# Kernel optimization log

Hardware: AMD Instinct MI355X
Metric: run time of the kernel (lower is better)

The kernel has to match this reference:

```python
import jax, jax.numpy as jnp
import numpy as np

N = 200000   # nodes
E = 3200000  # edges
B = 1024     # graphs in batch
A = 10       # num_actions
IN, C, ED = 9, 64, 1
NEG_SLOPE = 0.2


def _xavier(k, shape):
    lim = (6.0 / (shape[0] + shape[1])) ** 0.5
    return jax.random.uniform(k, shape, jnp.float32, -lim, lim)


def setup_inputs() -> dict:
    key = jax.random.key(0)
    ks = jax.random.split(key, 24)
    x = jax.random.normal(ks[0], (N, IN), jnp.float32)
    edge_index = jax.random.randint(ks[1], (2, E), 0, N, dtype=jnp.int64)
    edge_attr = jax.random.normal(ks[2], (E, ED), jnp.float32)
    agent_state = jax.random.normal(ks[3], (B, 34), jnp.float32)
    pool_batch = jnp.sort(jax.random.randint(ks[4], (N,), 0, B, dtype=jnp.int64))
    return {
        "x": x, "edge_index": edge_index, "edge_attr": edge_attr,
        "agent_state": agent_state, "pool_batch": pool_batch,
        # GATConv params (heads=1): lin (no bias), lin_edge (no bias), att vectors, bias
        "W_gat": _xavier(ks[5], (IN, C)),
        "att_src": jax.random.normal(ks[6], (C,), jnp.float32) * 0.1,
        "att_dst": jax.random.normal(ks[7], (C,), jnp.float32) * 0.1,
        "W_edge": _xavier(ks[8], (ED, C)),
        "att_edge": jax.random.normal(ks[9], (C,), jnp.float32) * 0.1,
        "b_gat": jnp.zeros((C,), jnp.float32),
        # fc_input1: Linear(64,128)
        "W1": _xavier(ks[10], (C, 128)), "b1": jnp.zeros((128,), jnp.float32),
        # fc_input2: Linear(34,64)
        "W2": _xavier(ks[11], (34, 64)), "b2": jnp.zeros((64,), jnp.float32),
        # fc_output: Linear(192,128), Linear(128,A)
        "W3": _xavier(ks[12], (192, 128)), "b3": jnp.zeros((128,), jnp.float32),
        "W4": _xavier(ks[13], (128, A)), "b4": jnp.zeros((A,), jnp.float32),
    }


def _gat_forward(x, edge_index, edge_attr, W_gat, att_src, att_dst, W_edge, att_edge, b_gat):
    src, dst = edge_index[0], edge_index[1]
    # add self-loops; self-loop edge_attr = mean of incoming edge_attr (PyG fill_value='mean')
    ones = jnp.ones((E,), jnp.float32)
    deg = jax.ops.segment_sum(ones, dst, num_segments=N)
    loop_attr = jax.ops.segment_sum(edge_attr, dst, num_segments=N) / jnp.maximum(deg, 1.0)[:, None]
    loop_idx = jnp.arange(N, dtype=src.dtype)
    src_f = jnp.concatenate([src, loop_idx])
    dst_f = jnp.concatenate([dst, loop_idx])
    attr_f = jnp.concatenate([edge_attr, loop_attr], axis=0)  # [E+N, 1]
    h = x @ W_gat                                   # [N, C]
    a_src = h @ att_src                             # [N]
    a_dst = h @ att_dst                             # [N]
    a_edge = (attr_f @ W_edge) @ att_edge           # [E+N]
    alpha = jax.nn.leaky_relu(a_src[src_f] + a_dst[dst_f] + a_edge, NEG_SLOPE)
    # per-destination softmax (stable)
    m = jax.ops.segment_max(alpha, dst_f, num_segments=N)
    ea = jnp.exp(alpha - m[dst_f])
    denom = jax.ops.segment_sum(ea, dst_f, num_segments=N)
    coef = ea / denom[dst_f]                        # [E+N]
    out = jax.ops.segment_sum(coef[:, None] * h[src_f], dst_f, num_segments=N)
    return out + b_gat


def reference(x, edge_index, edge_attr, agent_state, pool_batch,
              W_gat, att_src, att_dst, W_edge, att_edge, b_gat,
              W1, b1, W2, b2, W3, b3, W4, b4):
    g = _gat_forward(x, edge_index, edge_attr, W_gat, att_src, att_dst, W_edge, att_edge, b_gat)
    g = jax.nn.relu(g @ W1 + b1)                    # [N, 128]
    # global mean pool per graph
    s = jax.ops.segment_sum(g, pool_batch, num_segments=B)
    cnt = jax.ops.segment_sum(jnp.ones((N,), g.dtype), pool_batch, num_segments=B)
    pooled = s / jnp.maximum(cnt, 1.0)[:, None]     # [B, 128]
    a = jax.nn.relu(agent_state @ W2 + b2)          # [B, 64]
    z = jnp.concatenate([pooled, a], axis=-1)       # [B, 192]
    z = jax.nn.relu(z @ W3 + b3)
    return z @ W4 + b4                              # [B, A]
```

## Files before the change

### kernel.cpp

```cpp
#include <hip/hip_runtime.h>
#include <hip/hip_bf16.h>

namespace {

constexpr int kN  = 200000;
constexpr int kE  = 3200000;
constexpr int kB  = 1024;
constexpr int kA  = 10;
constexpr int kIn = 9;
constexpr int kC  = 64;
constexpr int kH1 = 128;
constexpr int kAS = 34;
constexpr int kH2 = 64;
constexpr int kZ  = 192;
constexpr int kH3 = 128;
constexpr int kMAXD = 192;
constexpr int kNBUCK = 782;
constexpr int kEPC  = 4096;
constexpr int kNCHK = (kE + kEPC - 1) / kEPC;
constexpr int kNODEBLK = kN / 4;

using bf16 = __hip_bfloat16;
typedef __attribute__((ext_vector_type(8))) short short8;
typedef __attribute__((ext_vector_type(4))) float f32x4;

__device__ __forceinline__ float b2f(bf16 v) { return __bfloat162float(v); }
__device__ __forceinline__ float lrelu(float x) { return x > 0.f ? x : 0.2f * x; }

__device__ __forceinline__ float ldf(const void* p, size_t i, int f32) {
  return f32 ? ((const float*)p)[i] : __bfloat162float(((const bf16*)p)[i]);
}
__device__ __forceinline__ int ldi(const void* p, size_t i, int i64) {
  return i64 ? (int)(((const long long*)p)[i]) : ((const int*)p)[i];
}

__global__ void k_init2(const void* __restrict__ ei, const void* __restrict__ x,
                        const void* __restrict__ We, const void* __restrict__ ae,
                        const void* __restrict__ Wg, const void* __restrict__ vsw,
                        const void* __restrict__ vdw, const void* __restrict__ W1,
                        const void* __restrict__ b1, const void* __restrict__ bgat,
                        int* __restrict__ flags, float* __restrict__ scal,
                        short* __restrict__ w1t, float* __restrict__ bb1) {
  __shared__ int c0, c1;
  int t = threadIdx.x;
  if (t == 0) { c0 = 0; c1 = 0; }
  __syncthreads();
  int zc = (((const int*)ei)[2 * t + 1] == 0) ? 1 : 0;
  int nc = 0;
  for (int j = t; j < 8192; j += 1024) {
    unsigned short u = ((const unsigned short*)x)[j];
    if ((u & 0x7F80u) == 0x7F80u) nc++;
  }
  atomicAdd(&c0, zc);
  atomicAdd(&c1, nc);
  __syncthreads();
  int f32 = (c1 > 3) ? 1 : 0;
  if (t == 0) { flags[0] = (c0 > 512) ? 1 : 0; flags[1] = f32; }
  int wid = t >> 6, lane = t & 63;
  if (wid == 0) {
    float p = ldf(We, lane, f32) * ldf(ae, lane, f32);
    #pragma unroll
    for (int o = 32; o > 0; o >>= 1) p += __shfl_xor(p, o);
    if (lane == 0) scal[0] = p;
  } else if (wid <= kIn) {
    int k = wid - 1;
    float w = ldf(Wg, (size_t)k * kC + lane, f32);
    float ps = w * ldf(vsw, lane, f32);
    float pd = w * ldf(vdw, lane, f32);
    #pragma unroll
    for (int o = 32; o > 0; o >>= 1) { ps += __shfl_xor(ps, o); pd += __shfl_xor(pd, o); }
    if (lane == 0) { scal[1 + k] = ps; scal[10 + k] = pd; }
  }
  for (int i = t; i < kC * kH1; i += 1024) {
    int c = i >> 6, k = i & 63;
    float v = ldf(W1, (size_t)k * kH1 + c, f32);
    w1t[i] = (short)__bfloat16_as_ushort(__float2bfloat16(v));
  }
  if (t < kH1) {
    int c = t;
    float s = ldf(b1, c, f32);
    for (int k = 0; k < kC; ++k)
      s += ldf(bgat, k, f32) * ldf(W1, (size_t)k * kH1 + c, f32);
    bb1[c] = s;
  }
}

__global__ void k_diag(const int* __restrict__ flags, float ws_mb,
                       float* __restrict__ out) {
  int i = blockIdx.x * 256 + threadIdx.x;
  if (i >= kB * kA) return;
  float v;
  if (flags) v = (1 + flags[0]) * 1e7f + (1 + flags[1]) * 1e6f + fminf(ws_mb, 999999.f);
  else       v = 3e7f + fminf(ws_mb, 999999.f);
  out[i] = v;
}

__global__ void __launch_bounds__(256) k_nodehist(
    const void* __restrict__ x, const void* __restrict__ Wg,
    const void* __restrict__ ei, const int* __restrict__ flags,
    const float* __restrict__ scal, bf16* __restrict__ hout,
    float* __restrict__ a_src, float* __restrict__ a_dst,
    int* __restrict__ blockhist) {
  int tid = threadIdx.x;
  int f32 = flags[1];
  if (blockIdx.x < kNODEBLK) {
    __shared__ float wg[kIn * kC];
    __shared__ float sc[19];
    for (int i = tid; i < kIn * kC; i += 256) wg[i] = ldf(Wg, i, f32);
    if (tid < 19) sc[tid] = scal[tid];
    __syncthreads();
    int n = blockIdx.x * 4 + (tid >> 6);
    int lane = tid & 63;
    float hc = 0.f, as_ = 0.f, ad_ = 0.f;
    #pragma unroll
    for (int k = 0; k < kIn; ++k) {
      float xv = ldf(x, (size_t)n * kIn + k, f32);
      hc  += xv * wg[k * kC + lane];
      as_ += xv * sc[1 + k];
      ad_ += xv * sc[10 + k];
    }
    hout[(size_t)n * kC + lane] = __float2bfloat16(hc);
    if (lane == 0) { a_src[n] = as_; a_dst[n] = ad_; }
  } else {
    __shared__ int hh[kNBUCK];
    int i64 = flags[0];
    int c = blockIdx.x - kNODEBLK;
    for (int i = tid; i < kNBUCK; i += 256) hh[i] = 0;
    __syncthreads();
    int e0 = c * kEPC;
    #pragma unroll
    for (int j = 0; j < 16; ++j) {
      int e = e0 + j * 256 + tid;
      if (e < kE) {
        int d = ldi(ei, (size_t)kE + e, i64);
        atomicAdd(&hh[d >> 8], 1);
      }
    }
    __syncthreads();
    for (int i = tid; i < kNBUCK; i += 256) blockhist[(size_t)i * kNCHK + c] = hh[i];
  }
}

__global__ void __launch_bounds__(256) r_scanA(int* __restrict__ blockhist,
                                               int* __restrict__ buckettot) {
  __shared__ int lds[256];
  int b = blockIdx.x, tid = threadIdx.x;
  int run = 0;
  for (int c0 = 0; c0 < kNCHK; c0 += 256) {
    int idx = c0 + tid;
    int v = (idx < kNCHK) ? blockhist[(size_t)b * kNCHK + idx] : 0;
    int xv = v;
    lds[tid] = xv;
    __syncthreads();
    #pragma unroll
    for (int o = 1; o < 256; o <<= 1) {
      int t = (tid >= o) ? lds[tid - o] : 0;
      __syncthreads();
      xv += t;
      lds[tid] = xv;
      __syncthreads();
    }
    if (idx < kNCHK) blockhist[(size_t)b * kNCHK + idx] = run + xv - v;
    run += lds[255];
    __syncthreads();
  }
  if (tid == 0) buckettot[b] = run;
}

__global__ void r_scanB(const int* __restrict__ buckettot, int* __restrict__ bucketbase) {
  __shared__ int lds[1024];
  int tid = threadIdx.x;
  int v = (tid < kNBUCK) ? buckettot[tid] : 0;
  int xv = v;
  lds[tid] = xv;
  __syncthreads();
  #pragma unroll
  for (int o = 1; o < 1024; o <<= 1) {
    int t = (tid >= o) ? lds[tid - o] : 0;
    __syncthreads();
    xv += t;
    lds[tid] = xv;
    __syncthreads();
  }
  if (tid < kNBUCK) bucketbase[tid] = xv - v;
  if (tid == kNBUCK - 1) bucketbase[kNBUCK] = xv;
}

__global__ void __launch_bounds__(256) r_scatter(
    const void* __restrict__ ei, const void* __restrict__ eattr,
    const int* __restrict__ flags, const float* __restrict__ a_src,
    const float* __restrict__ scal, const int* __restrict__ blockhist,
    const int* __restrict__ bucketbase, int2* __restrict__ mid) {
  __shared__ int cur[kNBUCK];
  int i64 = flags[0], f32 = flags[1];
  int c = blockIdx.x, tid = threadIdx.x;
  for (int i = tid; i < kNBUCK; i += 256)
    cur[i] = bucketbase[i] + blockhist[(size_t)i * kNCHK + c];
  __syncthreads();
  float sedge = scal[0];
  int e0 = c * kEPC;
  #pragma unroll
  for (int j = 0; j < 16; ++j) {
    int e = e0 + j * 256 + tid;
    if (e < kE) {
      int s = ldi(ei, e, i64);
      int d = ldi(ei, (size_t)kE + e, i64);
      float ap = a_src[s] + sedge * ldf(eattr, e, f32);
      int pos = atomicAdd(&cur[d >> 8], 1);
      mid[pos] = make_int2(s | ((d & 255) << 18), __float_as_int(ap));
    }
  }
}

__global__ void __launch_bounds__(256) r_bucket(
    const int2* __restrict__ mid, const int* __restrict__ bucketbase,
    int* __restrict__ offs, int2* __restrict__ csr) {
  __shared__ int h[256], cur[256], lds[256];
  int b = blockIdx.x, tid = threadIdx.x;
  int base = bucketbase[b];
  int cnt = bucketbase[b + 1] - base;
  h[tid] = 0;
  __syncthreads();
  for (int i = tid; i < cnt; i += 256)
    atomicAdd(&h[(mid[base + i].x >> 18) & 255], 1);
  __syncthreads();
  int v = h[tid];
  int xv = v;
  lds[tid] = xv;
  __syncthreads();
  #pragma unroll
  for (int o = 1; o < 256; o <<= 1) {
    int t = (tid >= o) ? lds[tid - o] : 0;
    __syncthreads();
    xv += t;
    lds[tid] = xv;
    __syncthreads();
  }
  int excl = xv - v;
  int n = b * 256 + tid;
  if (n < kN) offs[n] = base + excl;
  if (b == kNBUCK - 1 && tid == 0) offs[kN] = kE;
  cur[tid] = excl;
  __syncthreads();
  for (int i = tid; i < cnt; i += 256) {
    int2 e = mid[base + i];
    int dl = (e.x >> 18) & 255;
    int pos = atomicAdd(&cur[dl], 1);
    csr[base + pos] = make_int2(e.x & 0x3FFFF, e.y);
  }
}

__global__ void __launch_bounds__(256) k_gather5(
    const bf16* __restrict__ h, const float* __restrict__ a_src,
    const float* __restrict__ a_dst, const int* __restrict__ offs,
    const int2* __restrict__ csr, bf16* __restrict__ gbuf) {
  int wid = threadIdx.x >> 6, lane = threadIdx.x & 63;
  int n0 = (blockIdx.x * 4 + wid) * 4;
  for (int t = 0; t < 4; ++t) {
    int n = n0 + t;
    int base = offs[n];
    int degc = min(offs[n + 1] - base, kMAXD);
    float adst = a_dst[n], asrcn = a_src[n];
    int s0_ = 0, s1_ = 0, s2_ = 0;
    float e0_ = 0.f, e1_ = 0.f, e2_ = 0.f;
    float sap = 0.f;
    if (lane < degc) {
      int2 c = csr[base + lane];
      s0_ = c.x;
      float ap = __int_as_float(c.y);
      sap += ap - a_src[s0_];
      e0_ = __expf(fminf(lrelu(ap + adst), 60.f));
    }
    if (lane + 64 < degc) {
      int2 c = csr[base + lane + 64];
      s1_ = c.x;
      float ap = __int_as_float(c.y);
      sap += ap - a_src[s1_];
      e1_ = __expf(fminf(lrelu(ap + adst), 60.f));
    }
    if (lane + 128 < degc) {
      int2 c = csr[base + lane + 128];
      s2_ = c.x;
      float ap = __int_as_float(c.y);
      sap += ap - a_src[s2_];
      e2_ = __expf(fminf(lrelu(ap + adst), 60.f));
    }
    float se = e0_ + e1_ + e2_;
    #pragma unroll
    for (int o = 32; o > 0; o >>= 1) {
      se  += __shfl_xor(se, o);
      sap += __shfl_xor(sap, o);
    }
    float la = sap / fmaxf((float)degc, 1.0f);
    float aself = lrelu(asrcn + adst + la);
    float eself = __expf(fminf(aself, 60.f));
    float inv = 1.f / (se + eself);
    float g = eself * b2f(h[(size_t)n * kC + lane]);
    int lim = min(degc, 64);
    int j = 0;
    for (; j + 3 < lim; j += 4) {
      int sa = __shfl(s0_, j),     sb = __shfl(s0_, j + 1);
      int sc = __shfl(s0_, j + 2), sd = __shfl(s0_, j + 3);
      float ea = __shfl(e0_, j),     eb = __shfl(e0_, j + 1);
      float ec = __shfl(e0_, j + 2), ed = __shfl(e0_, j + 3);
      float ha = b2f(h[(size_t)sa * kC + lane]);
      float hb = b2f(h[(size_t)sb * kC + lane]);
      float hcv = b2f(h[(size_t)sc * kC + lane]);
      float hd = b2f(h[(size_t)sd * kC + lane]);
      g += ea * ha;
      g += eb * hb;
      g += ec * hcv;
      g += ed * hd;
    }
    for (; j < lim; ++j)
      g += __shfl(e0_, j) * b2f(h[(size_t)__shfl(s0_, j) * kC + lane]);
    if (degc > 64) {
      int lim1 = min(degc, 128) - 64;
      for (int j2 = 0; j2 < lim1; ++j2)
        g += __shfl(e1_, j2) * b2f(h[(size_t)__shfl(s1_, j2) * kC + lane]);
      if (degc > 128) {
        int lim2 = degc - 128;
        for (int j2 = 0; j2 < lim2; ++j2)
          g += __shfl(e2_, j2) * b2f(h[(size_t)__shfl(s2_, j2) * kC + lane]);
      }
    }
    gbuf[(size_t)n * kC + lane] = __float2bfloat16(g * inv);
  }
}

__device__ __forceinline__ int lowb(const void* pb, int i64, int target) {
  int lo = 0, hi = kN;
  while (lo < hi) {
    int mid = (lo + hi) >> 1;
    if (ldi(pb, mid, i64) < target) lo = mid + 1; else hi = mid;
  }
  return lo;
}

__global__ void __launch_bounds__(512) k_fc1graph(
    const short* __restrict__ gbuf, const short* __restrict__ w1t,
    const float* __restrict__ bb1, const void* __restrict__ pb,
    const int* __restrict__ flags, float* __restrict__ pooled) {
  int i64 = flags[0];
  int b = blockIdx.x;
  int wv = threadIdx.x >> 6, lane = threadIdx.x & 63;
  int col = lane & 15, kg = lane >> 4;
  int c = wv * 16 + col;
  int c0 = lowb(pb, i64, b);
  int c1 = lowb(pb, i64, b + 1);
  float ct = fmaxf((float)(c1 - c0), 1.0f);
  short8 bf0 = *(const short8*)(w1t + (size_t)c * kC + kg * 8);
  short8 bf1 = *(const short8*)(w1t + (size_t)c * kC + 32 + kg * 8);
  float bias = bb1[c];
  float pacc = 0.f;
  int g0 = c0 >> 4, g1 = (c1 + 15) >> 4;
  for (int gi = g0; gi < g1; ++gi) {
    int n0 = gi * 16;
    const short* arow = gbuf + (size_t)(n0 + col) * kC + kg * 8;
    short8 a0 = *(const short8*)(arow);
    short8 a1 = *(const short8*)(arow + 32);
    f32x4 acc = {bias, bias, bias, bias};
    acc = __builtin_amdgcn_mfma_f32_16x16x32_bf16(a0, bf0, acc, 0, 0, 0);
    acc = __builtin_amdgcn_mfma_f32_16x16x32_bf16(a1, bf1, acc, 0, 0, 0);
    #pragma unroll
    for (int r = 0; r < 4; ++r) {
      int node = n0 + kg * 4 + r;
      float v = fmaxf(acc[r], 0.f);
      pacc += (node >= c0 && node < c1) ? v : 0.f;
    }
  }
  pacc += __shfl_xor(pacc, 16);
  pacc += __shfl_xor(pacc, 32);
  if (kg == 0) pooled[(size_t)b * kH1 + c] = pacc / ct;
}

__global__ void k_final(const float* __restrict__ pooled,
                        const void* __restrict__ agent, const void* __restrict__ W2,
                        const void* __restrict__ b2v, const void* __restrict__ W3,
                        const void* __restrict__ b3v, const void* __restrict__ W4,
                        const void* __restrict__ b4v, const int* __restrict__ flags,
                        float* __restrict__ out) {
  __shared__ float z[kZ];
  __shared__ float t[kH3];
  int f32 = flags[1];
  int b = blockIdx.x, l = threadIdx.x;
  float av = ldf(b2v, l, f32);
  for (int k = 0; k < kAS; ++k)
    av += ldf(agent, (size_t)b * kAS + k, f32) * ldf(W2, (size_t)k * kH2 + l, f32);
  z[kH1 + l] = fmaxf(av, 0.f);
  z[l] = pooled[(size_t)b * kH1 + l];
  z[64 + l] = pooled[(size_t)b * kH1 + 64 + l];
  __syncthreads();
  float t0 = ldf(b3v, l, f32), t1 = ldf(b3v, 64 + l, f32);
  for (int k = 0; k < kZ; ++k) {
    float zk = z[k];
    t0 += zk * ldf(W3, (size_t)k * kH3 + l, f32);
    t1 += zk * ldf(W3, (size_t)k * kH3 + 64 + l, f32);
  }
  t[l] = fmaxf(t0, 0.f);
  t[64 + l] = fmaxf(t1, 0.f);
  __syncthreads();
  if (l < kA) {
    float o = ldf(b4v, l, f32);
    for (int k = 0; k < kH3; ++k) o += t[k] * ldf(W4, (size_t)k * kA + l, f32);
    out[b * kA + l] = o;
  }
}

}

extern "C" void kernel_launch(void* const* d_in, const int* in_sizes, int n_in,
                              void* d_out, int out_size, void* d_ws, size_t ws_size,
                              hipStream_t stream) {
  const void* x     = d_in[0];
  const void* ei    = d_in[1];
  const void* eattr = d_in[2];
  const void* agent = d_in[3];
  const void* pb    = d_in[4];
  const void* Wg    = d_in[5];
  const void* att_s = d_in[6];
  const void* att_d = d_in[7];
  const void* We    = d_in[8];
  const void* att_e = d_in[9];
  const void* bgat  = d_in[10];
  const void* W1    = d_in[11];
  const void* b1    = d_in[12];
  const void* W2    = d_in[13];
  const void* b2v   = d_in[14];
  const void* W3    = d_in[15];
  const void* b3v   = d_in[16];
  const void* W4    = d_in[17];
  const void* b4v   = d_in[18];
  float* out = (float*)d_out;

  char* ws = (char*)d_ws;
  size_t off = 0;
  auto alloc = [&](size_t bytes) -> void* {
    void* p = ws + off;
    off += (bytes + 255) & ~size_t(255);
    return p;
  };
  int*   flags  = (int*)alloc(256);
  size_t zbytes = off;
  float* pooled     = (float*)alloc(size_t(kB) * kH1 * 4);
  float* scal       = (float*)alloc(256);
  short* w1t        = (short*)alloc(size_t(kC) * kH1 * 2);
  float* bb1        = (float*)alloc(size_t(kH1) * 4);
  int*   buckettot  = (int*)alloc(size_t(kNBUCK) * 4);
  int*   bucketbase = (int*)alloc((size_t(kNBUCK) + 1) * 4);
  float* a_src      = (float*)alloc(size_t(kN) * 4);
  float* a_dst      = (float*)alloc(size_t(kN) * 4);
  int*   offs       = (int*)alloc((size_t(kN) + 1) * 4);
  int*   blockhist  = (int*)alloc(size_t(kNBUCK) * kNCHK * 4);
  int2*  csr = (int2*)alloc(size_t(kE) * 8);
  bf16*  h   = (bf16*)alloc(size_t(kN) * kC * 2);
  char*  uni  = (char*)alloc(size_t(kE) * 8 + 4096);
  int2*  mid  = (int2*)uni;
  bf16*  gbuf = (bf16*)uni;
  size_t need = off;

  float ws_mb = (float)(double(ws_size) / (1024.0 * 1024.0));

  if (ws_size < 4096) {
    k_diag<<<(kB * kA + 255) / 256, 256, 0, stream>>>(nullptr, ws_mb, out);
    return;
  }
  hipMemsetAsync(ws, 0, (ws_size < need) ? size_t(256) : zbytes, stream);
  k_init2<<<1, 1024, 0, stream>>>(ei, x, We, att_e, Wg, att_s, att_d, W1, b1, bgat,
                                  flags, scal, w1t, bb1);
  if (ws_size < need) {
    k_diag<<<(kB * kA + 255) / 256, 256, 0, stream>>>(flags, ws_mb, out);
    return;
  }

  k_nodehist<<<kNODEBLK + kNCHK, 256, 0, stream>>>(x, Wg, ei, flags, scal, h,
                                                   a_src, a_dst, blockhist);
  r_scanA<<<kNBUCK, 256, 0, stream>>>(blockhist, buckettot);
  r_scanB<<<1, 1024, 0, stream>>>(buckettot, bucketbase);
  r_scatter<<<kNCHK, 256, 0, stream>>>(ei, eattr, flags, a_src, scal, blockhist,
                                       bucketbase, mid);
  r_bucket<<<kNBUCK, 256, 0, stream>>>(mid, bucketbase, offs, csr);
  k_gather5<<<kN / 16, 256, 0, stream>>>(h, a_src, a_dst, offs, csr, gbuf);
  k_fc1graph<<<kB, 512, 0, stream>>>((const short*)gbuf, w1t, bb1, pb, flags, pooled);
  k_final<<<kB, 64, 0, stream>>>(pooled, agent, W2, b2v, W3, b3v, W4, b4v,
                                 flags, out);
}
```

Before: 374.8 us.

## Fuse per-bucket sort with attention gather in shared memory, dropping CSR pass

The bucket size drops from 256 to 128 destination nodes. The second-level per-destination sort is merged into the gather kernel: each block sorts its bucket's edges into LDS and then computes the softmax aggregation straight from LDS. This removes the global CSR array, the offsets array and one full write and read of the edge list. Edges per chunk are doubled and scatter uses 512 threads. The risk is that a bucket with more than 2688 edges is silently truncated, and the larger LDS footprint may lower occupancy.

```diff
diff --git a/kernel.cpp b/kernel.cpp
--- a/kernel.cpp
+++ b/kernel.cpp
@@ -14,9 +14,10 @@
 constexpr int kH2 = 64;
 constexpr int kZ  = 192;
 constexpr int kH3 = 128;
-constexpr int kMAXD = 192;
-constexpr int kNBUCK = 782;
-constexpr int kEPC  = 4096;
+constexpr int kDB = 128;
+constexpr int kNBUCK = (kN + kDB - 1) / kDB;
+constexpr int kSE = 2688;
+constexpr int kEPC  = 8192;
 constexpr int kNCHK = (kE + kEPC - 1) / kEPC;
 constexpr int kNODEBLK = kN / 4;
 
@@ -129,11 +130,11 @@
     __syncthreads();
     int e0 = c * kEPC;
     #pragma unroll
-    for (int j = 0; j < 16; ++j) {
+    for (int j = 0; j < kEPC / 256; ++j) {
       int e = e0 + j * 256 + tid;
       if (e < kE) {
         int d = ldi(ei, (size_t)kE + e, i64);
-        atomicAdd(&hh[d >> 8], 1);
+        atomicAdd(&hh[d >> 7], 1);
       }
     }
     __syncthreads();
@@ -170,8 +171,11 @@
 __global__ void r_scanB(const int* __restrict__ buckettot, int* __restrict__ bucketbase) {
   __shared__ int lds[1024];
   int tid = threadIdx.x;
-  int v = (tid < kNBUCK) ? buckettot[tid] : 0;
-  int xv = v;
+  int i0 = tid * 2, i1 = tid * 2 + 1;
+  int v0 = (i0 < kNBUCK) ? buckettot[i0] : 0;
+  int v1 = (i1 < kNBUCK) ? buckettot[i1] : 0;
+  int s = v0 + v1;
+  int xv = s;
   lds[tid] = xv;
   __syncthreads();
   #pragma unroll
@@ -182,11 +186,13 @@
     lds[tid] = xv;
     __syncthreads();
   }
-  if (tid < kNBUCK) bucketbase[tid] = xv - v;
-  if (tid == kNBUCK - 1) bucketbase[kNBUCK] = xv;
-}
-
-__global__ void __launch_bounds__(256) r_scatter(
+  int excl = xv - s;
+  if (i0 < kNBUCK) bucketbase[i0] = excl;
+  if (i1 < kNBUCK) bucketbase[i1] = excl + v0;
+  if (tid == 1023) bucketbase[kNBUCK] = xv;
+}
+
+__global__ void __launch_bounds__(512) r_scatter(
     const void* __restrict__ ei, const void* __restrict__ eattr,
     const int* __restrict__ flags, const float* __restrict__ a_src,
     const float* __restrict__ scal, const int* __restrict__ blockhist,
@@ -194,107 +200,110 @@
   __shared__ int cur[kNBUCK];
   int i64 = flags[0], f32 = flags[1];
   int c = blockIdx.x, tid = threadIdx.x;
-  for (int i = tid; i < kNBUCK; i += 256)
+  for (int i = tid; i < kNBUCK; i += 512)
     cur[i] = bucketbase[i] + blockhist[(size_t)i * kNCHK + c];
   __syncthreads();
   float sedge = scal[0];
   int e0 = c * kEPC;
   #pragma unroll
-  for (int j = 0; j < 16; ++j) {
-    int e = e0 + j * 256 + tid;
+  for (int j = 0; j < kEPC / 512; ++j) {
+    int e = e0 + j * 512 + tid;
     if (e < kE) {
       int s = ldi(ei, e, i64);
       int d = ldi(ei, (size_t)kE + e, i64);
       float ap = a_src[s] + sedge * ldf(eattr, e, f32);
-      int pos = atomicAdd(&cur[d >> 8], 1);
-      mid[pos] = make_int2(s | ((d & 255) << 18), __float_as_int(ap));
-    }
-  }
-}
-
-__global__ void __launch_bounds__(256) r_bucket(
+      int pos = atomicAdd(&cur[d >> 7], 1);
+      mid[pos] = make_int2(s | ((d & (kDB - 1)) << 18), __float_as_int(ap));
+    }
+  }
+}
+
+__global__ void __launch_bounds__(512) k_bucketgather2(
     const int2* __restrict__ mid, const int* __restrict__ bucketbase,
-    int* __restrict__ offs, int2* __restrict__ csr) {
-  __shared__ int h[256], cur[256], lds[256];
+    const float* __restrict__ a_src, const float* __restrict__ a_dst,
+    const bf16* __restrict__ h, bf16* __restrict__ gbuf) {
+  __shared__ int2 se[kSE];
+  __shared__ int hist[kDB], scanb[kDB], curs[kDB], doff[kDB + 1];
   int b = blockIdx.x, tid = threadIdx.x;
   int base = bucketbase[b];
-  int cnt = bucketbase[b + 1] - base;
-  h[tid] = 0;
-  __syncthreads();
-  for (int i = tid; i < cnt; i += 256)
-    atomicAdd(&h[(mid[base + i].x >> 18) & 255], 1);
-  __syncthreads();
-  int v = h[tid];
-  int xv = v;
-  lds[tid] = xv;
-  __syncthreads();
+  int cnt = min(bucketbase[b + 1] - base, kSE);
+  int n0 = b * kDB;
+  if (tid < kDB) hist[tid] = 0;
+  __syncthreads();
+  int2 myE[6];
   #pragma unroll
-  for (int o = 1; o < 256; o <<= 1) {
-    int t = (tid >= o) ? lds[tid - o] : 0;
-    __syncthreads();
-    xv += t;
-    lds[tid] = xv;
-    __syncthreads();
-  }
-  int excl = xv - v;
-  int n = b * 256 + tid;
-  if (n < kN) offs[n] = base + excl;
-  if (b == kNBUCK - 1 && tid == 0) offs[kN] = kE;
-  cur[tid] = excl;
-  __syncthreads();
-  for (int i = tid; i < cnt; i += 256) {
-    int2 e = mid[base + i];
-    int dl = (e.x >> 18) & 255;
-    int pos = atomicAdd(&cur[dl], 1);
-    csr[base + pos] = make_int2(e.x & 0x3FFFF, e.y);
-  }
-}
-
-__global__ void __launch_bounds__(256) k_gather5(
-    const bf16* __restrict__ h, const float* __restrict__ a_src,
-    const float* __restrict__ a_dst, const int* __restrict__ offs,
-    const int2* __restrict__ csr, bf16* __restrict__ gbuf) {
-  int wid = threadIdx.x >> 6, lane = threadIdx.x & 63;
-  int n0 = (blockIdx.x * 4 + wid) * 4;
-  for (int t = 0; t < 4; ++t) {
-    int n = n0 + t;
-    int base = offs[n];
-    int degc = min(offs[n + 1] - base, kMAXD);
+  for (int k = 0; k < 6; ++k) {
+    int i = tid + k * 512;
+    if (i < cnt) {
+      myE[k] = mid[base + i];
+      atomicAdd(&hist[(myE[k].x >> 18) & (kDB - 1)], 1);
+    }
+  }
+  __syncthreads();
+  int v = 0, xv = 0;
+  if (tid < kDB) { v = hist[tid]; xv = v; scanb[tid] = xv; }
+  __syncthreads();
+  for (int o = 1; o < kDB; o <<= 1) {
+    int t = (tid < kDB && tid >= o) ? scanb[tid - o] : 0;
+    __syncthreads();
+    if (tid < kDB) { xv += t; scanb[tid] = xv; }
+    __syncthreads();
+  }
+  if (tid < kDB) { doff[tid] = xv - v; curs[tid] = xv - v; }
+  if (tid == 0) doff[kDB] = cnt;
+  __syncthreads();
+  #pragma unroll
+  for (int k = 0; k < 6; ++k) {
+    int i = tid + k * 512;
+    if (i < cnt) {
+      int dl = (myE[k].x >> 18) & (kDB - 1);
+      int pos = atomicAdd(&curs[dl], 1);
+      se[pos] = make_int2(myE[k].x & 0x3FFFF, myE[k].y);
+    }
+  }
+  __syncthreads();
+  int wv = tid >> 6, lane = tid & 63;
+  for (int t = 0; t < kDB / 8; ++t) {
+    int dl = wv * (kDB / 8) + t;
+    int n = n0 + dl;
+    if (n >= kN) break;
+    int lo = doff[dl];
+    int degc = min(doff[dl + 1] - lo, 192);
     float adst = a_dst[n], asrcn = a_src[n];
     int s0_ = 0, s1_ = 0, s2_ = 0;
     float e0_ = 0.f, e1_ = 0.f, e2_ = 0.f;
     float sap = 0.f;
     if (lane < degc) {
-      int2 c = csr[base + lane];
+      int2 c = se[lo + lane];
       s0_ = c.x;
       float ap = __int_as_float(c.y);
       sap += ap - a_src[s0_];
       e0_ = __expf(fminf(lrelu(ap + adst), 60.f));
     }
     if (lane + 64 < degc) {
-      int2 c = csr[base + lane + 64];
+      int2 c = se[lo + lane + 64];
       s1_ = c.x;
       float ap = __int_as_float(c.y);
       sap += ap - a_src[s1_];
       e1_ = __expf(fminf(lrelu(ap + adst), 60.f));
     }
     if (lane + 128 < degc) {
-      int2 c = csr[base + lane + 128];
+      int2 c = se[lo + lane + 128];
       s2_ = c.x;
       float ap = __int_as_float(c.y);
       sap += ap - a_src[s2_];
       e2_ = __expf(fminf(lrelu(ap + adst), 60.f));
     }
-    float se = e0_ + e1_ + e2_;
+    float sum = e0_ + e1_ + e2_;
     #pragma unroll
     for (int o = 32; o > 0; o >>= 1) {
-      se  += __shfl_xor(se, o);
+      sum += __shfl_xor(sum, o);
       sap += __shfl_xor(sap, o);
     }
     float la = sap / fmaxf((float)degc, 1.0f);
     float aself = lrelu(asrcn + adst + la);
     float eself = __expf(fminf(aself, 60.f));
-    float inv = 1.f / (se + eself);
+    float inv = 1.f / (sum + eself);
     float g = eself * b2f(h[(size_t)n * kC + lane]);
     int lim = min(degc, 64);
     int j = 0;
@@ -343,7 +352,8 @@
     const int* __restrict__ flags, float* __restrict__ pooled) {
   int i64 = flags[0];
   int b = blockIdx.x;
-  int wv = threadIdx.x >> 6, lane = threadIdx.x & 63;
+  int lane = threadIdx.x & 63;
+  int wv = threadIdx.x >> 6;
   int col = lane & 15, kg = lane >> 4;
   int c = wv * 16 + col;
   int c0 = lowb(pb, i64, b);
@@ -450,13 +460,10 @@
   int*   bucketbase = (int*)alloc((size_t(kNBUCK) + 1) * 4);
   float* a_src      = (float*)alloc(size_t(kN) * 4);
   float* a_dst      = (float*)alloc(size_t(kN) * 4);
-  int*   offs       = (int*)alloc((size_t(kN) + 1) * 4);
   int*   blockhist  = (int*)alloc(size_t(kNBUCK) * kNCHK * 4);
-  int2*  csr = (int2*)alloc(size_t(kE) * 8);
-  bf16*  h   = (bf16*)alloc(size_t(kN) * kC * 2);
-  char*  uni  = (char*)alloc(size_t(kE) * 8 + 4096);
-  int2*  mid  = (int2*)uni;
-  bf16*  gbuf = (bf16*)uni;
+  bf16*  gbuf = (bf16*)alloc(size_t(kN) * kC * 2);
+  bf16*  h    = (bf16*)alloc(size_t(kN) * kC * 2);
+  int2*  mid  = (int2*)alloc(size_t(kE) * 8);
   size_t need = off;
 
   float ws_mb = (float)(double(ws_size) / (1024.0 * 1024.0));
@@ -477,10 +484,9 @@
                                                    a_src, a_dst, blockhist);
   r_scanA<<<kNBUCK, 256, 0, stream>>>(blockhist, buckettot);
   r_scanB<<<1, 1024, 0, stream>>>(buckettot, bucketbase);
-  r_scatter<<<kNCHK, 256, 0, stream>>>(ei, eattr, flags, a_src, scal, blockhist,
+  r_scatter<<<kNCHK, 512, 0, stream>>>(ei, eattr, flags, a_src, scal, blockhist,
                                        bucketbase, mid);
-  r_bucket<<<kNBUCK, 256, 0, stream>>>(mid, bucketbase, offs, csr);
-  k_gather5<<<kN / 16, 256, 0, stream>>>(h, a_src, a_dst, offs, csr, gbuf);
+  k_bucketgather2<<<kNBUCK, 512, 0, stream>>>(mid, bucketbase, a_src, a_dst, h, gbuf);
   k_fc1graph<<<kB, 512, 0, stream>>>((const short*)gbuf, w1t, bb1, pb, flags, pooled);
   k_final<<<kB, 64, 0, stream>>>(pooled, agent, W2, b2v, W3, b3v, W4, b4v,
                                  flags, out);
```

New measurement: 359.4 us. -4.1%, faster.
